# Kernel tuning notes

Measured on AMD Instinct MI355X. Metric: run time of the kernel, lower is better.

Reference implementation:

```python
import jax, jax.numpy as jnp
import numpy as np

NUM_POINTS = 1_000_000
WINDOW = 8                      # 2^3 corner stencil for linear shape functions in 3D
GRID = (128, 128, 128)
NUM_CELLS = GRID[0] * GRID[1] * GRID[2]
CELL = 1.0 / 64.0
INV_CELL = 64.0
ORIGIN = jnp.zeros((3,), dtype=jnp.float32)
# forward_window: the 8 corner offsets of the enclosing cell
FWD_WINDOW = jnp.array([[i, j, k] for i in (0, 1) for j in (0, 1) for k in (0, 1)],
                       dtype=jnp.int32)  # [8,3]


def setup_inputs() -> dict:
    key = jax.random.key(0)
    k1, k2, k3 = jax.random.split(key, 3)
    domain = GRID[0] * CELL
    # keep particles one cell away from the boundary so all stencil hashes are in range
    pos = jax.random.uniform(k1, (NUM_POINTS, 3), dtype=jnp.float32) * (domain - 2 * CELL) + CELL
    vel = jax.random.normal(k2, (NUM_POINTS, 3), dtype=jnp.float32)
    mass = jax.random.uniform(k3, (NUM_POINTS,), dtype=jnp.float32) * 1e-3 + 1e-4
    return {"position_stack": pos, "velocity_stack": vel, "mass_stack": mass}


def reference(position_stack, velocity_stack, mass_stack):
    # ---- get_interactions: gather particle pos, hash into grid, shape functions ----
    rel = (position_stack - ORIGIN) * INV_CELL               # [N,3] position in cell units
    base = jnp.floor(rel)                                    # [N,3]
    grid_pos = base[:, None, :] + FWD_WINDOW[None, :, :].astype(rel.dtype)  # [N,8,3]
    dist = rel[:, None, :] - grid_pos                        # [N,8,3], each dim in (-1,1)

    gp = grid_pos.astype(jnp.int32)
    # get_hash, dim==3: pos[2] + pos[0]*grid[2] + pos[1]*grid[2]*grid[0]
    intr_hash = gp[..., 2] + gp[..., 0] * GRID[2] + gp[..., 1] * (GRID[2] * GRID[0])  # [N,8]

    # linear shape function: N = prod_d (1 - |x_d|); grad scaled by inv_cell_size
    w = 1.0 - jnp.abs(dist)                                  # [N,8,3]
    shapef = w[..., 0] * w[..., 1] * w[..., 2]               # [N,8]
    valid = (intr_hash >= 0) & (intr_hash < NUM_CELLS)
    shapef = jnp.where(valid, shapef, 0.0)

    g0 = -jnp.sign(dist[..., 0]) * w[..., 1] * w[..., 2]
    g1 = -jnp.sign(dist[..., 1]) * w[..., 0] * w[..., 2]
    g2 = -jnp.sign(dist[..., 2]) * w[..., 0] * w[..., 1]
    shapef_grad = jnp.stack([g0, g1, g2], axis=-1) * INV_CELL  # [N,8,3]
    shapef_grad = jnp.where(valid[..., None], shapef_grad, 0.0)

    # intr_dist_padded = -dist * cell_size (kept implicitly via dist; used in APIC-style p2g)
    # ---- p2g scatter (vmap_intr_scatter semantics): mass & momentum to grid nodes ----
    h_flat = jnp.clip(intr_hash, 0, NUM_CELLS - 1).reshape(-1)  # [N*8]
    sm = shapef * mass_stack[:, None]                           # [N,8]
    node_mass = jax.ops.segment_sum(sm.reshape(-1), h_flat, num_segments=NUM_CELLS)   # [C]
    mom = sm[..., None] * velocity_stack[:, None, :]            # [N,8,3]
    node_mom = jax.ops.segment_sum(mom.reshape(-1, 3), h_flat, num_segments=NUM_CELLS)  # [C,3]

    return jnp.concatenate([node_mass[:, None], node_mom], axis=1)  # [C,4]
```

## Files before the change

kernel.cpp:

```cpp
#include <hip/hip_runtime.h>
#include <hip/hip_fp16.h>


#define GRID_DIM   128
#define NUM_CELLS  (GRID_DIM * GRID_DIM * GRID_DIM)
#define INV_CELL   64.0f
#define OVF_MAX    65536
#define SCAN_BLKS  2048

#define TDIM       16
#define NTILES     (TDIM * TDIM * TDIM)
#define NXCD       8
#define XCAP       48
#define MAXCAP     3
#define NSC        729
#define PLANE      736

typedef float floatx4 __attribute__((ext_vector_type(4)));

__device__ __forceinline__ int cell_id(int ix, int iy, int iz) {
    return iz + ix * GRID_DIM + iy * (GRID_DIM * GRID_DIM);
}

__device__ __forceinline__ unsigned int q16(float f) {
    int q = (int)(f * 65536.0f + 0.5f);
    return (unsigned int)min(q, 65535);
}
__device__ __forceinline__ unsigned int f2h(float f) {
    return (unsigned int)__half_as_ushort(__float2half(f));
}
__device__ __forceinline__ float h2f(unsigned int b) {
    return __half2float(__ushort_as_half((unsigned short)(b & 0xffffu)));
}

__global__ __launch_bounds__(256) void xcd_place_kernel(
    const float* __restrict__ pos, const float* __restrict__ vel,
    const float* __restrict__ mass, unsigned int* __restrict__ tile_cnt,
    uint4* __restrict__ lists, int* __restrict__ ovf_cnt,
    int* __restrict__ ovf_list, int n)
{
    int i = blockIdx.x * 256 + threadIdx.x;
    if (i >= n) return;
    int xcd = blockIdx.x & (NXCD - 1);
    float px = __builtin_nontemporal_load(&pos[3 * i + 0]);
    float py = __builtin_nontemporal_load(&pos[3 * i + 1]);
    float pz = __builtin_nontemporal_load(&pos[3 * i + 2]);
    float rx = px * INV_CELL, ry = py * INV_CELL, rz = pz * INV_CELL;
    float bx = floorf(rx), by = floorf(ry), bz = floorf(rz);
    float fx = rx - bx, fy = ry - by, fz = rz - bz;
    int ix = min(max((int)bx, 0), GRID_DIM - 1);
    int iy = min(max((int)by, 0), GRID_DIM - 1);
    int iz = min(max((int)bz, 0), GRID_DIM - 1);
    int tile = (iz >> 3) | ((ix >> 3) << 4) | ((iy >> 3) << 8);
    int sub = (xcd << 12) | tile;
    unsigned int s = atomicAdd(&tile_cnt[sub], 1u);
    if (s < (unsigned int)XCAP) {
        float m  = __builtin_nontemporal_load(&mass[i]);
        float vx = __builtin_nontemporal_load(&vel[3 * i + 0]);
        float vy = __builtin_nontemporal_load(&vel[3 * i + 1]);
        float vz = __builtin_nontemporal_load(&vel[3 * i + 2]);
        unsigned int lid = (unsigned int)((iz & 7) | ((ix & 7) << 3)
                                                   | ((iy & 7) << 6));
        uint4 r;
        r.x = q16(fx) | (q16(fy) << 16);
        r.y = q16(fz) | (f2h(m) << 16);
        r.z = f2h(vx) | (f2h(vy) << 16);
        r.w = f2h(vz) | (lid << 16);
        lists[(size_t)sub * XCAP + (int)s] = r;
    } else {
        int o = atomicAdd(ovf_cnt, 1);
        if (o < OVF_MAX) ovf_list[o] = i;
    }
}

__global__ __launch_bounds__(512) void xcd_gather_kernel(
    const uint4* __restrict__ lists, const unsigned int* __restrict__ tile_cnt,
    float4* __restrict__ out)
{
    __shared__ unsigned int cnt_s[NSC];
    __shared__ unsigned int rec_s[4 * MAXCAP * PLANE];
    __shared__ float nacc[4 * 512];
    __shared__ unsigned int seg_off[65];
    __shared__ unsigned int seg_cnt[64];

    int tid = threadIdx.x;
    int swz = (blockIdx.x & 7) * 512 + (blockIdx.x >> 3);
    int bz = swz & 15;
    int bx = (swz >> 4) & 15;
    int by = swz >> 8;
    int g0x = bx * 8, g0y = by * 8, g0z = bz * 8;

    for (int sc = tid; sc < NSC; sc += 512) cnt_s[sc] = 0;
    nacc[tid] = 0.0f; nacc[512 + tid] = 0.0f;
    nacc[1024 + tid] = 0.0f; nacc[1536 + tid] = 0.0f;

    if (tid < 64) {
        int xcd = tid & 7, lt = tid >> 3;
        int ltz = lt & 1, ltx = (lt >> 1) & 1, lty = lt >> 2;
        int tz_ = bz - 1 + ltz, tx_ = bx - 1 + ltx, ty_ = by - 1 + lty;
        unsigned int c = 0;
        if ((tz_ >= 0) & (tx_ >= 0) & (ty_ >= 0)) {
            int tile = tz_ + (tx_ << 4) + (ty_ << 8);
            c = min(tile_cnt[(xcd << 12) | tile], (unsigned int)XCAP);
        }
        seg_cnt[tid] = c;
    }
    __syncthreads();
    if (tid == 0) {
        unsigned int run = 0;
        for (int s = 0; s < 64; ++s) { seg_off[s] = run; run += seg_cnt[s]; }
        seg_off[64] = run;
    }
    __syncthreads();
    int R = (int)seg_off[64];

    for (int r = tid; r < R; r += 512) {
        int s = 0;
        #pragma unroll
        for (int step = 32; step >= 1; step >>= 1)
            if (seg_off[s + step] <= (unsigned int)r) s += step;
        int xcd = s & 7, lt = s >> 3;
        int ltz = lt & 1, ltx = (lt >> 1) & 1, lty = lt >> 2;
        int tz_ = bz - 1 + ltz, tx_ = bx - 1 + ltx, ty_ = by - 1 + lty;
        int tile = tz_ + (tx_ << 4) + (ty_ << 8);
        int j = r - (int)seg_off[s];
        uint4 rec = lists[(size_t)((xcd << 12) | tile) * XCAP + j];
        unsigned int lid = rec.w >> 16;
        int cz = tz_ * 8 + (int)(lid & 7u);
        int cx = tx_ * 8 + (int)((lid >> 3) & 7u);
        int cy = ty_ * 8 + (int)(lid >> 6);
        int uz = cz - (g0z - 1), ux = cx - (g0x - 1), uy = cy - (g0y - 1);
        if (((unsigned)uz < 9u) & ((unsigned)ux < 9u) & ((unsigned)uy < 9u)) {
            int sc = uy * 81 + ux * 9 + uz;
            unsigned int j2 = atomicAdd(&cnt_s[sc], 1u);
            if (j2 < MAXCAP) {
                rec_s[(0 * MAXCAP + j2) * PLANE + sc] = rec.x;
                rec_s[(1 * MAXCAP + j2) * PLANE + sc] = rec.y;
                rec_s[(2 * MAXCAP + j2) * PLANE + sc] = rec.z;
                rec_s[(3 * MAXCAP + j2) * PLANE + sc] = rec.w;
            } else {
                float fx = (float)(rec.x & 0xffffu) * (1.0f / 65536.0f);
                float fy = (float)(rec.x >> 16)     * (1.0f / 65536.0f);
                float fz = (float)(rec.y & 0xffffu) * (1.0f / 65536.0f);
                float m  = h2f(rec.y >> 16);
                float vx = h2f(rec.z), vy = h2f(rec.z >> 16), vz = h2f(rec.w);
                #pragma unroll
                for (int oy = 0; oy < 2; ++oy)
                #pragma unroll
                for (int ox = 0; ox < 2; ++ox)
                #pragma unroll
                for (int oz = 0; oz < 2; ++oz) {
                    int pz = cz + oz - g0z;
                    int px = cx + ox - g0x;
                    int py = cy + oy - g0y;
                    if (((unsigned)pz < 8u) & ((unsigned)px < 8u) &
                        ((unsigned)py < 8u)) {
                        float w = (ox ? fx : 1.0f - fx) *
                                  (oy ? fy : 1.0f - fy) *
                                  (oz ? fz : 1.0f - fz);
                        float sm = w * m;
                        int idx = py * 64 + px * 8 + pz;
                        atomicAdd(&nacc[0 * 512 + idx], sm);
                        atomicAdd(&nacc[1 * 512 + idx], sm * vx);
                        atomicAdd(&nacc[2 * 512 + idx], sm * vy);
                        atomicAdd(&nacc[3 * 512 + idx], sm * vz);
                    }
                }
            }
        }
    }
    __syncthreads();

    int tz = tid & 7, tx = (tid >> 3) & 7, ty = tid >> 6;
    float a0 = nacc[tid], a1 = nacc[512 + tid];
    float a2 = nacc[1024 + tid], a3 = nacc[1536 + tid];

    #pragma unroll
    for (int dy = 0; dy < 2; ++dy) {
        #pragma unroll
        for (int dx = 0; dx < 2; ++dx) {
            int scb = (ty + dy) * 81 + (tx + dx) * 9 + tz;
            #pragma unroll
            for (int dz = 0; dz < 2; ++dz) {
                int sc = scb + dz;
                int cnt = min((int)cnt_s[sc], MAXCAP);
                for (int j = 0; j < cnt; ++j) {
                    unsigned r0 = rec_s[(0 * MAXCAP + j) * PLANE + sc];
                    unsigned r1 = rec_s[(1 * MAXCAP + j) * PLANE + sc];
                    unsigned r2 = rec_s[(2 * MAXCAP + j) * PLANE + sc];
                    unsigned r3 = rec_s[(3 * MAXCAP + j) * PLANE + sc];
                    float fx = (float)(r0 & 0xffffu) * (1.0f / 65536.0f);
                    float fy = (float)(r0 >> 16)     * (1.0f / 65536.0f);
                    float fz = (float)(r1 & 0xffffu) * (1.0f / 65536.0f);
                    float wx = dx ? (1.0f - fx) : fx;
                    float wy = dy ? (1.0f - fy) : fy;
                    float wz = dz ? (1.0f - fz) : fz;
                    float sm = wx * wy * wz * h2f(r1 >> 16);
                    a0 += sm;
                    a1 += sm * h2f(r2);
                    a2 += sm * h2f(r2 >> 16);
                    a3 += sm * h2f(r3);
                }
            }
        }
    }
    int id = (g0z + tz) + (g0x + tx) * GRID_DIM
           + (g0y + ty) * (GRID_DIM * GRID_DIM);
    floatx4 v = { a0, a1, a2, a3 };
    __builtin_nontemporal_store(v, (floatx4*)&out[id]);
}

__global__ __launch_bounds__(256) void fixup_kernel(
    const float* __restrict__ pos, const float* __restrict__ vel,
    const float* __restrict__ mass, const int* __restrict__ ovf_cnt,
    const int* __restrict__ ovf_list, float* __restrict__ out)
{
    int total = min(*ovf_cnt, OVF_MAX);
    for (int k = blockIdx.x * 256 + threadIdx.x; k < total; k += gridDim.x * 256) {
        int i = ovf_list[k];
        float px = pos[3 * i + 0] * INV_CELL;
        float py = pos[3 * i + 1] * INV_CELL;
        float pz = pos[3 * i + 2] * INV_CELL;
        float bx = floorf(px), by = floorf(py), bz = floorf(pz);
        float fx = px - bx, fy = py - by, fz = pz - bz;
        int ix = (int)bx, iy = (int)by, iz = (int)bz;
        float m = mass[i];
        float vx = vel[3 * i + 0], vy = vel[3 * i + 1], vz = vel[3 * i + 2];
        float wx[2] = { 1.0f - fx, fx }, wy[2] = { 1.0f - fy, fy }, wz[2] = { 1.0f - fz, fz };
        #pragma unroll
        for (int a = 0; a < 2; ++a)
            #pragma unroll
            for (int b = 0; b < 2; ++b)
                #pragma unroll
                for (int c = 0; c < 2; ++c) {
                    int h = cell_id(ix + a, iy + b, iz + c);
                    bool valid = (h >= 0) && (h < NUM_CELLS);
                    int hc = min(max(h, 0), NUM_CELLS - 1);
                    float s = valid ? (wx[a] * wy[b] * wz[c]) : 0.0f;
                    float sm = s * m;
                    float* cell = out + 4 * (size_t)hc;
                    atomicAdd(cell + 0, sm);
                    atomicAdd(cell + 1, sm * vx);
                    atomicAdd(cell + 2, sm * vy);
                    atomicAdd(cell + 3, sm * vz);
                }
    }
}

__global__ __launch_bounds__(256) void s_hist_kernel(
    const float* __restrict__ pos, int* __restrict__ counts, int n)
{
    int i = blockIdx.x * 256 + threadIdx.x;
    if (i >= n) return;
    int ix = min(max((int)floorf(pos[3 * i + 0] * INV_CELL), 0), GRID_DIM - 1);
    int iy = min(max((int)floorf(pos[3 * i + 1] * INV_CELL), 0), GRID_DIM - 1);
    int iz = min(max((int)floorf(pos[3 * i + 2] * INV_CELL), 0), GRID_DIM - 1);
    atomicAdd(&counts[cell_id(ix, iy, iz)], 1);
}

__global__ __launch_bounds__(256) void s_scan_partials_kernel(
    const int* __restrict__ counts, int* __restrict__ partials)
{
    __shared__ int red[256];
    int t = threadIdx.x;
    int4 v = ((const int4*)counts)[blockIdx.x * 256 + t];
    red[t] = v.x + v.y + v.z + v.w;
    __syncthreads();
    for (int off = 128; off > 0; off >>= 1) {
        if (t < off) red[t] += red[t + off];
        __syncthreads();
    }
    if (t == 0) partials[blockIdx.x] = red[0];
}

__global__ __launch_bounds__(1024) void s_scan_tops_kernel(int* __restrict__ partials)
{
    __shared__ int s[1024];
    int t = threadIdx.x;
    int p0 = partials[2 * t], p1 = partials[2 * t + 1];
    int sum = p0 + p1;
    s[t] = sum;
    __syncthreads();
    for (int off = 1; off < 1024; off <<= 1) {
        int x = (t >= off) ? s[t - off] : 0;
        __syncthreads();
        s[t] += x;
        __syncthreads();
    }
    int excl = s[t] - sum;
    partials[2 * t] = excl;
    partials[2 * t + 1] = excl + p0;
}

__global__ __launch_bounds__(256) void s_scan_final_kernel(
    const int* __restrict__ counts, const int* __restrict__ partials,
    int* __restrict__ offsets, int* __restrict__ cursors)
{
    __shared__ int s[256];
    int t = threadIdx.x;
    int g = blockIdx.x * 256 + t;
    int4 v = ((const int4*)counts)[g];
    int sum = v.x + v.y + v.z + v.w;
    s[t] = sum;
    __syncthreads();
    for (int off = 1; off < 256; off <<= 1) {
        int x = (t >= off) ? s[t - off] : 0;
        __syncthreads();
        s[t] += x;
        __syncthreads();
    }
    int run = partials[blockIdx.x] + s[t] - sum;
    int4 o = make_int4(run, run + v.x, run + v.x + v.y, run + v.x + v.y + v.z);
    ((int4*)offsets)[g] = o;
    ((int4*)cursors)[g] = o;
}

__global__ __launch_bounds__(256) void s_binplace_kernel(
    const float* __restrict__ pos, const float* __restrict__ vel,
    const float* __restrict__ mass, int* __restrict__ cursors,
    float4* __restrict__ records, int n)
{
    int i = blockIdx.x * 256 + threadIdx.x;
    if (i >= n) return;
    float rx = pos[3 * i + 0] * INV_CELL;
    float ry = pos[3 * i + 1] * INV_CELL;
    float rz = pos[3 * i + 2] * INV_CELL;
    int ix = min(max((int)floorf(rx), 0), GRID_DIM - 1);
    int iy = min(max((int)floorf(ry), 0), GRID_DIM - 1);
    int iz = min(max((int)floorf(rz), 0), GRID_DIM - 1);
    int slot = atomicAdd(&cursors[cell_id(ix, iy, iz)], 1);
    records[2 * slot + 0] = make_float4(rx, ry, rz, mass[i]);
    records[2 * slot + 1] = make_float4(vel[3 * i + 0], vel[3 * i + 1],
                                        vel[3 * i + 2], 0.0f);
}

__global__ __launch_bounds__(256) void s_node_gather_kernel(
    const float4* __restrict__ records, const int* __restrict__ offsets,
    const int* __restrict__ cursors, float4* __restrict__ out)
{
    int id = blockIdx.x * 256 + threadIdx.x;
    int gz = id & (GRID_DIM - 1);
    int gx = (id >> 7) & (GRID_DIM - 1);
    int gy = id >> 14;
    float fgx = (float)gx, fgy = (float)gy, fgz = (float)gz;
    float a0 = 0.0f, a1 = 0.0f, a2 = 0.0f, a3 = 0.0f;
    int z0 = max(gz - 1, 0), y0 = max(gy - 1, 0), x0 = max(gx - 1, 0);
    for (int cy = y0; cy <= gy; ++cy) {
        for (int cx = x0; cx <= gx; ++cx) {
            int cb = cx * GRID_DIM + cy * (GRID_DIM * GRID_DIM);
            int beg = offsets[cb + z0];
            int end = cursors[cb + gz];
            for (int p = beg; p < end; ++p) {
                float4 r0 = records[2 * p + 0];
                float4 r1 = records[2 * p + 1];
                float w = (1.0f - fabsf(r0.x - fgx)) *
                          (1.0f - fabsf(r0.y - fgy)) *
                          (1.0f - fabsf(r0.z - fgz));
                float sm = w * r0.w;
                a0 += sm; a1 += sm * r1.x; a2 += sm * r1.y; a3 += sm * r1.z;
            }
        }
    }
    out[id] = make_float4(a0, a1, a2, a3);
}

__global__ __launch_bounds__(256) void p2g_scatter_kernel(
    const float* __restrict__ pos, const float* __restrict__ vel,
    const float* __restrict__ mass, float* __restrict__ out, int n)
{
    int i = blockIdx.x * blockDim.x + threadIdx.x;
    if (i >= n) return;
    float px = pos[3 * i + 0] * INV_CELL;
    float py = pos[3 * i + 1] * INV_CELL;
    float pz = pos[3 * i + 2] * INV_CELL;
    float bx = floorf(px), by = floorf(py), bz = floorf(pz);
    float fx = px - bx, fy = py - by, fz = pz - bz;
    int ix = (int)bx, iy = (int)by, iz = (int)bz;
    float m = mass[i];
    float vx = vel[3 * i + 0], vy = vel[3 * i + 1], vz = vel[3 * i + 2];
    float wx[2] = { 1.0f - fx, fx }, wy[2] = { 1.0f - fy, fy }, wz[2] = { 1.0f - fz, fz };
    #pragma unroll
    for (int a = 0; a < 2; ++a)
        #pragma unroll
        for (int b = 0; b < 2; ++b)
            #pragma unroll
            for (int c = 0; c < 2; ++c) {
                int h = cell_id(ix + a, iy + b, iz + c);
                bool valid = (h >= 0) && (h < NUM_CELLS);
                int hc = min(max(h, 0), NUM_CELLS - 1);
                float s = valid ? (wx[a] * wy[b] * wz[c]) : 0.0f;
                float sm = s * m;
                float* cell = out + 4 * (size_t)hc;
                atomicAdd(cell + 0, sm);
                atomicAdd(cell + 1, sm * vx);
                atomicAdd(cell + 2, sm * vy);
                atomicAdd(cell + 3, sm * vz);
            }
}

extern "C" void kernel_launch(void* const* d_in, const int* in_sizes, int n_in,
                              void* d_out, int out_size, void* d_ws, size_t ws_size,
                              hipStream_t stream) {
    const float* pos  = (const float*)d_in[0];
    const float* vel  = (const float*)d_in[1];
    const float* mass = (const float*)d_in[2];
    float* out = (float*)d_out;
    int n = in_sizes[2];
    int blocks = (n + 255) / 256;

    size_t x_off_lists = (size_t)NXCD * NTILES * 4;
    size_t x_off_ovf   = x_off_lists + (size_t)NXCD * NTILES * XCAP * 16;
    size_t need_xcd    = x_off_ovf + 256 + (size_t)OVF_MAX * 4;

    size_t s_off_offsets  = (size_t)NUM_CELLS * 4;
    size_t s_off_records  = s_off_offsets + (size_t)NUM_CELLS * 4;
    size_t s_off_partials = s_off_records + (size_t)n * 32;
    size_t need_sorted    = s_off_partials + (size_t)SCAN_BLKS * 4;

    if (ws_size >= need_xcd) {
        char* ws = (char*)d_ws;
        unsigned int* tile_cnt = (unsigned int*)ws;
        uint4* lists  = (uint4*)(ws + x_off_lists);
        int* ovf_cnt  = (int*)(ws + x_off_ovf);
        int* ovf_list = ovf_cnt + 64;

        (void)hipMemsetAsync(tile_cnt, 0, x_off_lists, stream);
        (void)hipMemsetAsync(ovf_cnt, 0, 4, stream);
        xcd_place_kernel<<<blocks, 256, 0, stream>>>(
            pos, vel, mass, tile_cnt, lists, ovf_cnt, ovf_list, n);
        xcd_gather_kernel<<<NTILES, 512, 0, stream>>>(
            lists, tile_cnt, (float4*)out);
        fixup_kernel<<<32, 256, 0, stream>>>(pos, vel, mass, ovf_cnt,
                                             ovf_list, out);
    } else if (ws_size >= need_sorted) {
        char* ws = (char*)d_ws;
        int* counts   = (int*)ws;
        int* offsets  = (int*)(ws + s_off_offsets);
        float4* records = (float4*)(ws + s_off_records);
        int* partials = (int*)(ws + s_off_partials);

        (void)hipMemsetAsync(counts, 0, (size_t)NUM_CELLS * 4, stream);
        s_hist_kernel<<<blocks, 256, 0, stream>>>(pos, counts, n);
        s_scan_partials_kernel<<<SCAN_BLKS, 256, 0, stream>>>(counts, partials);
        s_scan_tops_kernel<<<1, 1024, 0, stream>>>(partials);
        s_scan_final_kernel<<<SCAN_BLKS, 256, 0, stream>>>(counts, partials,
                                                           offsets, counts);
        s_binplace_kernel<<<blocks, 256, 0, stream>>>(pos, vel, mass, counts,
                                                      records, n);
        s_node_gather_kernel<<<NUM_CELLS / 256, 256, 0, stream>>>(
            records, offsets, counts, (float4*)out);
    } else {
        (void)hipMemsetAsync(out, 0, (size_t)out_size * sizeof(float), stream);
        p2g_scatter_kernel<<<blocks, 256, 0, stream>>>(pos, vel, mass, out, n);
    }
}
```

Measured before the change: 179.7 us.

## Use finer 4^3 binning tiles and restructure gather shared-memory staging

```diff
diff --git a/kernel.cpp b/kernel.cpp
--- a/kernel.cpp
+++ b/kernel.cpp
@@ -8,13 +8,14 @@
 #define OVF_MAX    65536
 #define SCAN_BLKS  2048
 
-#define TDIM       16
-#define NTILES     (TDIM * TDIM * TDIM)
+#define TDIM4      32
+#define NTILES4    (TDIM4 * TDIM4 * TDIM4)
 #define NXCD       8
-#define XCAP       48
+#define XCAP       16
 #define MAXCAP     3
-#define NSC        729
-#define PLANE      736
+#define NSEG       216
+#define NREC       2369
+#define EPAD(sc)   ((sc) * 3 + ((sc) >> 2))
 
 typedef float floatx4 __attribute__((ext_vector_type(4)));
 
@@ -39,37 +40,42 @@
     uint4* __restrict__ lists, int* __restrict__ ovf_cnt,
     int* __restrict__ ovf_list, int n)
 {
-    int i = blockIdx.x * 256 + threadIdx.x;
-    if (i >= n) return;
     int xcd = blockIdx.x & (NXCD - 1);
-    float px = __builtin_nontemporal_load(&pos[3 * i + 0]);
-    float py = __builtin_nontemporal_load(&pos[3 * i + 1]);
-    float pz = __builtin_nontemporal_load(&pos[3 * i + 2]);
-    float rx = px * INV_CELL, ry = py * INV_CELL, rz = pz * INV_CELL;
-    float bx = floorf(rx), by = floorf(ry), bz = floorf(rz);
-    float fx = rx - bx, fy = ry - by, fz = rz - bz;
-    int ix = min(max((int)bx, 0), GRID_DIM - 1);
-    int iy = min(max((int)by, 0), GRID_DIM - 1);
-    int iz = min(max((int)bz, 0), GRID_DIM - 1);
-    int tile = (iz >> 3) | ((ix >> 3) << 4) | ((iy >> 3) << 8);
-    int sub = (xcd << 12) | tile;
-    unsigned int s = atomicAdd(&tile_cnt[sub], 1u);
-    if (s < (unsigned int)XCAP) {
-        float m  = __builtin_nontemporal_load(&mass[i]);
-        float vx = __builtin_nontemporal_load(&vel[3 * i + 0]);
-        float vy = __builtin_nontemporal_load(&vel[3 * i + 1]);
-        float vz = __builtin_nontemporal_load(&vel[3 * i + 2]);
-        unsigned int lid = (unsigned int)((iz & 7) | ((ix & 7) << 3)
-                                                   | ((iy & 7) << 6));
-        uint4 r;
-        r.x = q16(fx) | (q16(fy) << 16);
-        r.y = q16(fz) | (f2h(m) << 16);
-        r.z = f2h(vx) | (f2h(vy) << 16);
-        r.w = f2h(vz) | (lid << 16);
-        lists[(size_t)sub * XCAP + (int)s] = r;
-    } else {
-        int o = atomicAdd(ovf_cnt, 1);
-        if (o < OVF_MAX) ovf_list[o] = i;
+    int i0 = blockIdx.x * 512 + threadIdx.x;
+    #pragma unroll
+    for (int k = 0; k < 2; ++k) {
+        int i = i0 + k * 256;
+        if (i < n) {
+            float px = __builtin_nontemporal_load(&pos[3 * i + 0]);
+            float py = __builtin_nontemporal_load(&pos[3 * i + 1]);
+            float pz = __builtin_nontemporal_load(&pos[3 * i + 2]);
+            float rx = px * INV_CELL, ry = py * INV_CELL, rz = pz * INV_CELL;
+            float bx = floorf(rx), by = floorf(ry), bz = floorf(rz);
+            float fx = rx - bx, fy = ry - by, fz = rz - bz;
+            int ix = min(max((int)bx, 0), GRID_DIM - 1);
+            int iy = min(max((int)by, 0), GRID_DIM - 1);
+            int iz = min(max((int)bz, 0), GRID_DIM - 1);
+            int tile = (iz >> 2) | ((ix >> 2) << 5) | ((iy >> 2) << 10);
+            int sub = (xcd << 15) | tile;
+            unsigned int s = atomicAdd(&tile_cnt[sub], 1u);
+            if (s < (unsigned int)XCAP) {
+                float m  = __builtin_nontemporal_load(&mass[i]);
+                float vx = __builtin_nontemporal_load(&vel[3 * i + 0]);
+                float vy = __builtin_nontemporal_load(&vel[3 * i + 1]);
+                float vz = __builtin_nontemporal_load(&vel[3 * i + 2]);
+                unsigned int lid = (unsigned int)((iz & 3) | ((ix & 3) << 2)
+                                                           | ((iy & 3) << 4));
+                uint4 r;
+                r.x = q16(fx) | (q16(fy) << 16);
+                r.y = q16(fz) | (f2h(m) << 16);
+                r.z = f2h(vx) | (f2h(vy) << 16);
+                r.w = f2h(vz) | (lid << 16);
+                lists[(size_t)sub * XCAP + (int)s] = r;
+            } else {
+                int o = atomicAdd(ovf_cnt, 1);
+                if (o < OVF_MAX) ovf_list[o] = i;
+            }
+        }
     }
 }
 
@@ -77,11 +83,14 @@
     const uint4* __restrict__ lists, const unsigned int* __restrict__ tile_cnt,
     float4* __restrict__ out)
 {
-    __shared__ unsigned int cnt_s[NSC];
-    __shared__ unsigned int rec_s[4 * MAXCAP * PLANE];
-    __shared__ float nacc[4 * 512];
-    __shared__ unsigned int seg_off[65];
-    __shared__ unsigned int seg_cnt[64];
+    __shared__ float4 recA[NREC];
+    __shared__ unsigned int recB[NREC];
+    __shared__ unsigned int cnt_s[729];
+    __shared__ unsigned short seg_off[218];
+    __shared__ int wtot[8];
+    __shared__ int ovf_n;
+    __shared__ short ovf_sc[64];
+    __shared__ uint4 ovf_rec[64];
 
     int tid = threadIdx.x;
     int swz = (blockIdx.x & 7) * 512 + (blockIdx.x >> 3);
@@ -89,91 +98,76 @@
     int bx = (swz >> 4) & 15;
     int by = swz >> 8;
     int g0x = bx * 8, g0y = by * 8, g0z = bz * 8;
-
-    for (int sc = tid; sc < NSC; sc += 512) cnt_s[sc] = 0;
-    nacc[tid] = 0.0f; nacc[512 + tid] = 0.0f;
-    nacc[1024 + tid] = 0.0f; nacc[1536 + tid] = 0.0f;
-
-    if (tid < 64) {
-        int xcd = tid & 7, lt = tid >> 3;
-        int ltz = lt & 1, ltx = (lt >> 1) & 1, lty = lt >> 2;
-        int tz_ = bz - 1 + ltz, tx_ = bx - 1 + ltx, ty_ = by - 1 + lty;
-        unsigned int c = 0;
+    int Tz0 = bz * 2 - 1, Tx0 = bx * 2 - 1, Ty0 = by * 2 - 1;
+
+    for (int s2 = tid; s2 < 729; s2 += 512) cnt_s[s2] = 0;
+    if (tid == 0) ovf_n = 0;
+
+    unsigned int c = 0;
+    if (tid < NSEG) {
+        int xcd = tid & 7, q = tid >> 3;
+        int ltz = q % 3, q2 = q / 3, ltx = q2 % 3, lty = q2 / 3;
+        int tz_ = Tz0 + ltz, tx_ = Tx0 + ltx, ty_ = Ty0 + lty;
         if ((tz_ >= 0) & (tx_ >= 0) & (ty_ >= 0)) {
-            int tile = tz_ + (tx_ << 4) + (ty_ << 8);
-            c = min(tile_cnt[(xcd << 12) | tile], (unsigned int)XCAP);
-        }
-        seg_cnt[tid] = c;
-    }
+            int tile = tz_ | (tx_ << 5) | (ty_ << 10);
+            c = min(tile_cnt[(xcd << 15) | tile], (unsigned int)XCAP);
+        }
+    }
+    unsigned int v = c;
+    #pragma unroll
+    for (int d = 1; d < 64; d <<= 1) {
+        unsigned int t = __shfl_up(v, d, 64);
+        if ((tid & 63) >= d) v += t;
+    }
+    if ((tid & 63) == 63) wtot[tid >> 6] = (int)v;
     __syncthreads();
     if (tid == 0) {
-        unsigned int run = 0;
-        for (int s = 0; s < 64; ++s) { seg_off[s] = run; run += seg_cnt[s]; }
-        seg_off[64] = run;
-    }
-    __syncthreads();
-    int R = (int)seg_off[64];
+        int run = 0;
+        #pragma unroll
+        for (int w2 = 0; w2 < 8; ++w2) { int t = wtot[w2]; wtot[w2] = run; run += t; }
+    }
+    __syncthreads();
+    if (tid <= NSEG)
+        seg_off[tid] = (unsigned short)((unsigned int)wtot[tid >> 6] + v - c);
+    __syncthreads();
+    int R = (int)seg_off[NSEG];
 
     for (int r = tid; r < R; r += 512) {
         int s = 0;
         #pragma unroll
-        for (int step = 32; step >= 1; step >>= 1)
-            if (seg_off[s + step] <= (unsigned int)r) s += step;
-        int xcd = s & 7, lt = s >> 3;
-        int ltz = lt & 1, ltx = (lt >> 1) & 1, lty = lt >> 2;
-        int tz_ = bz - 1 + ltz, tx_ = bx - 1 + ltx, ty_ = by - 1 + lty;
-        int tile = tz_ + (tx_ << 4) + (ty_ << 8);
+        for (int step = 128; step >= 1; step >>= 1)
+            if (s + step <= NSEG && (int)seg_off[s + step] <= r) s += step;
+        int xcd = s & 7, q = s >> 3;
+        int ltz = q % 3, q2 = q / 3, ltx = q2 % 3, lty = q2 / 3;
+        int tz_ = Tz0 + ltz, tx_ = Tx0 + ltx, ty_ = Ty0 + lty;
+        int tile = tz_ | (tx_ << 5) | (ty_ << 10);
         int j = r - (int)seg_off[s];
-        uint4 rec = lists[(size_t)((xcd << 12) | tile) * XCAP + j];
+        uint4 rec = lists[(size_t)((xcd << 15) | tile) * XCAP + j];
         unsigned int lid = rec.w >> 16;
-        int cz = tz_ * 8 + (int)(lid & 7u);
-        int cx = tx_ * 8 + (int)((lid >> 3) & 7u);
-        int cy = ty_ * 8 + (int)(lid >> 6);
+        int cz = tz_ * 4 + (int)(lid & 3u);
+        int cx = tx_ * 4 + (int)((lid >> 2) & 3u);
+        int cy = ty_ * 4 + (int)(lid >> 4);
         int uz = cz - (g0z - 1), ux = cx - (g0x - 1), uy = cy - (g0y - 1);
         if (((unsigned)uz < 9u) & ((unsigned)ux < 9u) & ((unsigned)uy < 9u)) {
             int sc = uy * 81 + ux * 9 + uz;
             unsigned int j2 = atomicAdd(&cnt_s[sc], 1u);
             if (j2 < MAXCAP) {
-                rec_s[(0 * MAXCAP + j2) * PLANE + sc] = rec.x;
-                rec_s[(1 * MAXCAP + j2) * PLANE + sc] = rec.y;
-                rec_s[(2 * MAXCAP + j2) * PLANE + sc] = rec.z;
-                rec_s[(3 * MAXCAP + j2) * PLANE + sc] = rec.w;
-            } else {
+                int e = EPAD(sc) + (int)j2;
                 float fx = (float)(rec.x & 0xffffu) * (1.0f / 65536.0f);
                 float fy = (float)(rec.x >> 16)     * (1.0f / 65536.0f);
                 float fz = (float)(rec.y & 0xffffu) * (1.0f / 65536.0f);
-                float m  = h2f(rec.y >> 16);
-                float vx = h2f(rec.z), vy = h2f(rec.z >> 16), vz = h2f(rec.w);
-                #pragma unroll
-                for (int oy = 0; oy < 2; ++oy)
-                #pragma unroll
-                for (int ox = 0; ox < 2; ++ox)
-                #pragma unroll
-                for (int oz = 0; oz < 2; ++oz) {
-                    int pz = cz + oz - g0z;
-                    int px = cx + ox - g0x;
-                    int py = cy + oy - g0y;
-                    if (((unsigned)pz < 8u) & ((unsigned)px < 8u) &
-                        ((unsigned)py < 8u)) {
-                        float w = (ox ? fx : 1.0f - fx) *
-                                  (oy ? fy : 1.0f - fy) *
-                                  (oz ? fz : 1.0f - fz);
-                        float sm = w * m;
-                        int idx = py * 64 + px * 8 + pz;
-                        atomicAdd(&nacc[0 * 512 + idx], sm);
-                        atomicAdd(&nacc[1 * 512 + idx], sm * vx);
-                        atomicAdd(&nacc[2 * 512 + idx], sm * vy);
-                        atomicAdd(&nacc[3 * 512 + idx], sm * vz);
-                    }
-                }
+                recA[e] = make_float4(fx, fy, fz, __uint_as_float(rec.z));
+                recB[e] = (rec.y >> 16) | (rec.w << 16);
+            } else {
+                int o = atomicAdd(&ovf_n, 1);
+                if (o < 64) { ovf_sc[o] = (short)sc; ovf_rec[o] = rec; }
             }
         }
     }
     __syncthreads();
 
     int tz = tid & 7, tx = (tid >> 3) & 7, ty = tid >> 6;
-    float a0 = nacc[tid], a1 = nacc[512 + tid];
-    float a2 = nacc[1024 + tid], a3 = nacc[1536 + tid];
+    float a0 = 0.0f, a1 = 0.0f, a2 = 0.0f, a3 = 0.0f;
 
     #pragma unroll
     for (int dy = 0; dy < 2; ++dy) {
@@ -184,30 +178,49 @@
             for (int dz = 0; dz < 2; ++dz) {
                 int sc = scb + dz;
                 int cnt = min((int)cnt_s[sc], MAXCAP);
+                int eb = EPAD(sc);
                 for (int j = 0; j < cnt; ++j) {
-                    unsigned r0 = rec_s[(0 * MAXCAP + j) * PLANE + sc];
-                    unsigned r1 = rec_s[(1 * MAXCAP + j) * PLANE + sc];
-                    unsigned r2 = rec_s[(2 * MAXCAP + j) * PLANE + sc];
-                    unsigned r3 = rec_s[(3 * MAXCAP + j) * PLANE + sc];
-                    float fx = (float)(r0 & 0xffffu) * (1.0f / 65536.0f);
-                    float fy = (float)(r0 >> 16)     * (1.0f / 65536.0f);
-                    float fz = (float)(r1 & 0xffffu) * (1.0f / 65536.0f);
-                    float wx = dx ? (1.0f - fx) : fx;
-                    float wy = dy ? (1.0f - fy) : fy;
-                    float wz = dz ? (1.0f - fz) : fz;
-                    float sm = wx * wy * wz * h2f(r1 >> 16);
+                    float4 A = recA[eb + j];
+                    unsigned int B = recB[eb + j];
+                    unsigned int w3 = __float_as_uint(A.w);
+                    float wx = dx ? (1.0f - A.x) : A.x;
+                    float wy = dy ? (1.0f - A.y) : A.y;
+                    float wz = dz ? (1.0f - A.z) : A.z;
+                    float sm = wx * wy * wz * h2f(B);
                     a0 += sm;
-                    a1 += sm * h2f(r2);
-                    a2 += sm * h2f(r2 >> 16);
-                    a3 += sm * h2f(r3);
+                    a1 += sm * h2f(w3);
+                    a2 += sm * h2f(w3 >> 16);
+                    a3 += sm * h2f(B >> 16);
                 }
             }
         }
     }
+
+    int no = min(ovf_n, 64);
+    for (int e2 = 0; e2 < no; ++e2) {
+        int sc = (int)ovf_sc[e2];
+        int uzv = sc % 9, t2 = sc / 9, uxv = t2 % 9, uyv = t2 / 9;
+        int ddz = uzv - tz, ddx = uxv - tx, ddy = uyv - ty;
+        if (((unsigned)ddz < 2u) & ((unsigned)ddx < 2u) & ((unsigned)ddy < 2u)) {
+            uint4 rec = ovf_rec[e2];
+            float fx = (float)(rec.x & 0xffffu) * (1.0f / 65536.0f);
+            float fy = (float)(rec.x >> 16)     * (1.0f / 65536.0f);
+            float fz = (float)(rec.y & 0xffffu) * (1.0f / 65536.0f);
+            float wx = ddx ? (1.0f - fx) : fx;
+            float wy = ddy ? (1.0f - fy) : fy;
+            float wz = ddz ? (1.0f - fz) : fz;
+            float sm = wx * wy * wz * h2f(rec.y >> 16);
+            a0 += sm;
+            a1 += sm * h2f(rec.z);
+            a2 += sm * h2f(rec.z >> 16);
+            a3 += sm * h2f(rec.w);
+        }
+    }
+
     int id = (g0z + tz) + (g0x + tx) * GRID_DIM
            + (g0y + ty) * (GRID_DIM * GRID_DIM);
-    floatx4 v = { a0, a1, a2, a3 };
-    __builtin_nontemporal_store(v, (floatx4*)&out[id]);
+    floatx4 vv = { a0, a1, a2, a3 };
+    __builtin_nontemporal_store(vv, (floatx4*)&out[id]);
 }
 
 __global__ __launch_bounds__(256) void fixup_kernel(
@@ -408,8 +421,8 @@
     int n = in_sizes[2];
     int blocks = (n + 255) / 256;
 
-    size_t x_off_lists = (size_t)NXCD * NTILES * 4;
-    size_t x_off_ovf   = x_off_lists + (size_t)NXCD * NTILES * XCAP * 16;
+    size_t x_off_lists = (size_t)NXCD * NTILES4 * 4;
+    size_t x_off_ovf   = x_off_lists + (size_t)NXCD * NTILES4 * XCAP * 16;
     size_t need_xcd    = x_off_ovf + 256 + (size_t)OVF_MAX * 4;
 
     size_t s_off_offsets  = (size_t)NUM_CELLS * 4;
@@ -426,9 +439,9 @@
 
         (void)hipMemsetAsync(tile_cnt, 0, x_off_lists, stream);
         (void)hipMemsetAsync(ovf_cnt, 0, 4, stream);
-        xcd_place_kernel<<<blocks, 256, 0, stream>>>(
+        xcd_place_kernel<<<(n + 511) / 512, 256, 0, stream>>>(
             pos, vel, mass, tile_cnt, lists, ovf_cnt, ovf_list, n);
-        xcd_gather_kernel<<<NTILES, 512, 0, stream>>>(
+        xcd_gather_kernel<<<NTILES4 / 8, 512, 0, stream>>>(
             lists, tile_cnt, (float4*)out);
         fixup_kernel<<<32, 256, 0, stream>>>(pos, vel, mass, ovf_cnt,
                                              ovf_list, out);
```

Result: faster. 175.7 us (-2.2%).
